# Kernel tuning notes

Hardware: AMD Instinct MI355X
Metric: run time of the kernel (lower is better)

The kernel has to match this reference:

```python
import jax, jax.numpy as jnp
import numpy as np

B, S, D, E, F, TOP_K = 2, 2048, 1024, 8, 4096, 2


def setup_inputs() -> dict:
    key = jax.random.key(0)
    k0, k1, k2, k3 = jax.random.split(key, 4)
    x = jax.random.normal(k0, (B, S, D), dtype=jnp.float32)
    gate_w = jax.random.normal(k1, (D, E), dtype=jnp.float32) * 0.02  # Linear(d_model, num_experts, bias=False)
    w1 = jax.random.normal(k2, (E, D, F), dtype=jnp.float32) * 0.02   # per-expert Linear(d_model, d_ff)
    b1 = jnp.zeros((E, F), dtype=jnp.float32)
    w2 = jax.random.normal(k3, (E, F, D), dtype=jnp.float32) * 0.02   # per-expert Linear(d_ff, d_model)
    b2 = jnp.zeros((E, D), dtype=jnp.float32)
    return {"x": x, "gate_w": gate_w, "w1": w1, "b1": b1, "w2": w2, "b2": b2}


def reference(x, gate_w, w1, b1, w2, b2):
    b, s, d = x.shape
    e = gate_w.shape[1]
    xf = x.reshape(-1, d)                       # [T, D], T = B*S
    t = xf.shape[0]

    # Router: top-k gate scores, softmax over the selected k scores only
    scores = xf @ gate_w                        # [T, E]
    top_v, top_i = jax.lax.top_k(scores, TOP_K)  # [T, K]
    probs = jax.nn.softmax(top_v, axis=-1)       # [T, K]

    # Combine weights per (token, expert); scatter-add of top-k probs.
    combine = jnp.zeros((t, e), dtype=xf.dtype).at[
        jnp.arange(t)[:, None], top_i
    ].add(probs)                                 # [T, E]

    # Dense grouped FFN over all experts (dropout=0 / eval mode -> identity).
    h = jax.nn.gelu(jnp.einsum('td,edf->etf', xf, w1) + b1[:, None, :],
                    approximate=False)           # [E, T, F]
    y = jnp.einsum('etf,efd->etd', h, w2) + b2[:, None, :]  # [E, T, D]

    # Weighted combine: tokens only receive output from their top-k experts.
    out = jnp.einsum('etd,te->td', y, combine)   # [T, D]
    return out.reshape(b, s, d)
```

## Files before the change

### kernel.cpp

```cpp
#include <hip/hip_runtime.h>
#include <math.h>

typedef __bf16 bf16;
typedef __bf16 bf16x8 __attribute__((ext_vector_type(8)));
typedef float f32x4 __attribute__((ext_vector_type(4)));

#define T_TOK 4096
#define D_DIM 1024
#define E_EXP 8
#define F_DIM 4096
#define BM 128
#define BN 128
#define BK 64
#define PAD_SLOTS 9216

__device__ __forceinline__ void gload16(const bf16* g, bf16* l) {
  __builtin_amdgcn_global_load_lds(
      (const __attribute__((address_space(1))) void*)g,
      (__attribute__((address_space(3))) void*)l, 16, 0, 0);
}

__global__ __launch_bounds__(64) void router_kernel(
    const float* __restrict__ x, const float* __restrict__ gw,
    int* __restrict__ eidx, float* __restrict__ pval, int* __restrict__ cnt)
{
  const int t = blockIdx.x;
  const int lane = threadIdx.x;
  const float* xr = x + (size_t)t * D_DIM;
  float s[E_EXP];
#pragma unroll
  for (int e = 0; e < E_EXP; ++e) s[e] = 0.f;
#pragma unroll
  for (int j = 0; j < D_DIM / 64; ++j) {
    const int d = lane * (D_DIM / 64) + j;
    const float xv = xr[d];
    const float* g = gw + (size_t)d * E_EXP;
#pragma unroll
    for (int e = 0; e < E_EXP; ++e) s[e] += xv * g[e];
  }
#pragma unroll
  for (int off = 32; off > 0; off >>= 1) {
#pragma unroll
    for (int e = 0; e < E_EXP; ++e) s[e] += __shfl_xor(s[e], off, 64);
  }
  if (lane == 0) {
    int i0 = 0;
#pragma unroll
    for (int e = 1; e < E_EXP; ++e) if (s[e] > s[i0]) i0 = e;
    int i1 = (i0 == 0) ? 1 : 0;
#pragma unroll
    for (int e = 0; e < E_EXP; ++e) if (e != i0 && s[e] > s[i1]) i1 = e;
    const float p1 = 1.f / (1.f + expf(s[i0] - s[i1]));
    eidx[2 * t] = i0;  eidx[2 * t + 1] = i1;
    pval[2 * t] = 1.f - p1;  pval[2 * t + 1] = p1;
    atomicAdd(&cnt[i0], 1);
    atomicAdd(&cnt[i1], 1);
  }
}

__global__ void prefix_kernel(const int* __restrict__ cnt, int* __restrict__ off,
                              int* __restrict__ cursor)
{
  if (blockIdx.x == 0 && threadIdx.x == 0) {
    int acc = 0;
    for (int e = 0; e < E_EXP; ++e) {
      off[e] = acc;
      cursor[e] = acc;
      acc += ((cnt[e] + BM - 1) / BM) * BM;
    }
    off[E_EXP] = acc;
  }
}

__global__ __launch_bounds__(256) void scatter_kernel(
    const int* __restrict__ eidx, const float* __restrict__ pval,
    int* __restrict__ cursor, int* __restrict__ tok_flat,
    float* __restrict__ prob_flat, int* __restrict__ slot_of)
{
  const int i = blockIdx.x * 256 + threadIdx.x;
  if (i < T_TOK * 2) {
    const int e = eidx[i];
    const int pos = atomicAdd(&cursor[e], 1);
    tok_flat[pos] = i >> 1;
    prob_flat[pos] = pval[i];
    slot_of[i] = pos;
  }
}

__global__ __launch_bounds__(256) void xcast_kernel(const float* __restrict__ x,
                                                    bf16* __restrict__ xb)
{
  const size_t i = (size_t)(blockIdx.x * 256 + threadIdx.x) * 8;
  const float4 a = *(const float4*)(x + i);
  const float4 b = *(const float4*)(x + i + 4);
  union { bf16 v[8]; int4 q; } u;
  u.v[0] = (bf16)a.x; u.v[1] = (bf16)a.y; u.v[2] = (bf16)a.z; u.v[3] = (bf16)a.w;
  u.v[4] = (bf16)b.x; u.v[5] = (bf16)b.y; u.v[6] = (bf16)b.z; u.v[7] = (bf16)b.w;
  *(int4*)(xb + i) = u.q;
}

__global__ __launch_bounds__(256) void wtrans_kernel(const float* __restrict__ src,
                                                     bf16* __restrict__ dst,
                                                     int R, int C)
{
  __shared__ float tile[64][68];
  const int e = blockIdx.z;
  const int r0 = blockIdx.y * 64;
  const int c0 = blockIdx.x * 64;
  const float* sp = src + (size_t)e * R * C;
  const int tr = threadIdx.x >> 4;
  const int tc = (threadIdx.x & 15) * 4;
#pragma unroll
  for (int p = 0; p < 4; ++p) {
    const int r = p * 16 + tr;
    const float4 v = *(const float4*)(sp + (size_t)(r0 + r) * C + c0 + tc);
    *(float4*)&tile[r][tc] = v;
  }
  __syncthreads();
  bf16* dp = dst + (size_t)e * C * R;
  const int oc = threadIdx.x & 31;
  const int orr = (threadIdx.x >> 5) * 8;
#pragma unroll
  for (int p = 0; p < 2; ++p) {
    const int c = p * 32 + oc;
    union { bf16 v[8]; int4 q; } u;
#pragma unroll
    for (int j = 0; j < 8; ++j) u.v[j] = (bf16)tile[orr + j][c];
    *(int4*)(dp + (size_t)(c0 + c) * R + r0 + orr) = u.q;
  }
}

template <int MODE>
__global__ __launch_bounds__(256) void gemm_kernel(
    const bf16* __restrict__ Abase, const bf16* __restrict__ BT,
    const float* __restrict__ bias, const int* __restrict__ cnt,
    const int* __restrict__ off, const int* __restrict__ tok_flat,
    const float* __restrict__ prob_flat, bf16* __restrict__ Hout,
    bf16* __restrict__ Yout)
{
  constexpr int K = (MODE == 0) ? 1024 : 4096;
  constexpr int N = (MODE == 0) ? 4096 : 1024;
  constexpr int NT = N / BN;

  const int b = blockIdx.x;
  const int nt = b % NT;
  const int mt = (b / NT) % 32;
  const int e  = b / (NT * 32);
  if (mt * BM >= cnt[e]) return;
  const int rowBase = off[e] + mt * BM;
  const int nBase = nt * BN;

  __shared__ bf16 sA[BM * BK];
  __shared__ bf16 sB[BN * BK];

  const int tid = threadIdx.x;
  const int lane = tid & 63;
  const int wid = tid >> 6;
  const int mW = (wid >> 1) * 64;
  const int nW = (wid & 1) * 64;

  const bf16* aptr[4];
  const bf16* bptr[4];
#pragma unroll
  for (int j = 0; j < 4; ++j) {
    const int r = wid * 32 + j * 8 + (lane >> 3);
    if (MODE == 0) {
      int tok = tok_flat[rowBase + r];
      if (tok < 0) tok = 0;
      aptr[j] = Abase + (size_t)tok * K + (lane & 7) * 8;
    } else {
      aptr[j] = Abase + (size_t)(rowBase + r) * K + (lane & 7) * 8;
    }
    bptr[j] = BT + ((size_t)e * N + nBase + r) * K + (lane & 7) * 8;
  }

  f32x4 acc[4][4];
#pragma unroll
  for (int m = 0; m < 4; ++m)
#pragma unroll
    for (int n = 0; n < 4; ++n) acc[m][n] = (f32x4){0.f, 0.f, 0.f, 0.f};

  for (int kt = 0; kt < K / BK; ++kt) {
#pragma unroll
    for (int j = 0; j < 4; ++j) {
      gload16(aptr[j] + kt * BK, &sA[(wid * 32 + j * 8) * BK]);
      gload16(bptr[j] + kt * BK, &sB[(wid * 32 + j * 8) * BK]);
    }
    __syncthreads();
#pragma unroll
    for (int ks = 0; ks < 2; ++ks) {
      const int kb = ks * 64 + ((lane >> 4) << 4);
      bf16x8 af[4], bfr[4];
#pragma unroll
      for (int m = 0; m < 4; ++m) {
        const int row = mW + m * 16 + (lane & 15);
        af[m] = *(const bf16x8*)((const char*)sA + row * 128 + kb);
      }
#pragma unroll
      for (int n = 0; n < 4; ++n) {
        const int row = nW + n * 16 + (lane & 15);
        bfr[n] = *(const bf16x8*)((const char*)sB + row * 128 + kb);
      }
#pragma unroll
      for (int m = 0; m < 4; ++m)
#pragma unroll
        for (int n = 0; n < 4; ++n)
          acc[m][n] = __builtin_amdgcn_mfma_f32_16x16x32_bf16(af[m], bfr[n], acc[m][n], 0, 0, 0);
    }
    __syncthreads();
  }

  const int col0 = nW + (lane & 15);
  const int rsub = (lane >> 4) * 4;
  if (MODE == 0) {
#pragma unroll
    for (int m = 0; m < 4; ++m) {
#pragma unroll
      for (int n = 0; n < 4; ++n) {
        const int colg = nBase + col0 + n * 16;
        const float bb = bias[e * N + colg];
#pragma unroll
        for (int r = 0; r < 4; ++r) {
          const int rowl = mW + m * 16 + rsub + r;
          float v = acc[m][n][r] + bb;
          v = 0.5f * v * (1.0f + erff(v * 0.70710678118f));
          Hout[(size_t)(rowBase + rowl) * F_DIM + colg] = (bf16)v;
        }
      }
    }
  } else {
#pragma unroll
    for (int m = 0; m < 4; ++m) {
#pragma unroll
      for (int r = 0; r < 4; ++r) {
        const int slot = rowBase + mW + m * 16 + rsub + r;
        const float p = prob_flat[slot];
#pragma unroll
        for (int n = 0; n < 4; ++n) {
          const int colg = nBase + col0 + n * 16;
          const float v = (acc[m][n][r] + bias[e * N + colg]) * p;
          Yout[(size_t)slot * D_DIM + colg] = (bf16)v;
        }
      }
    }
  }
}

__global__ __launch_bounds__(256) void combine_kernel(
    const bf16* __restrict__ y, const int* __restrict__ slot_of,
    float* __restrict__ out)
{
  const int i = blockIdx.x * 256 + threadIdx.x;
  const int t = i >> 7;
  const int dq = (i & 127) * 8;
  const int s0 = slot_of[2 * t];
  const int s1 = slot_of[2 * t + 1];
  const bf16x8 a = *(const bf16x8*)(y + (size_t)s0 * D_DIM + dq);
  const bf16x8 b = *(const bf16x8*)(y + (size_t)s1 * D_DIM + dq);
  float4 o0, o1;
  o0.x = (float)a[0] + (float)b[0];  o0.y = (float)a[1] + (float)b[1];
  o0.z = (float)a[2] + (float)b[2];  o0.w = (float)a[3] + (float)b[3];
  o1.x = (float)a[4] + (float)b[4];  o1.y = (float)a[5] + (float)b[5];
  o1.z = (float)a[6] + (float)b[6];  o1.w = (float)a[7] + (float)b[7];
  *(float4*)(out + (size_t)t * D_DIM + dq) = o0;
  *(float4*)(out + (size_t)t * D_DIM + dq + 4) = o1;
}

extern "C" void kernel_launch(void* const* d_in, const int* in_sizes, int n_in,
                              void* d_out, int out_size, void* d_ws, size_t ws_size,
                              hipStream_t stream) {
  const float* x      = (const float*)d_in[0];
  const float* gate_w = (const float*)d_in[1];
  const float* w1     = (const float*)d_in[2];
  const float* b1     = (const float*)d_in[3];
  const float* w2     = (const float*)d_in[4];
  const float* b2     = (const float*)d_in[5];
  float* out = (float*)d_out;

  char* ws = (char*)d_ws;
  size_t o = 0;
  bf16* xb  = (bf16*)(ws + o); o += (size_t)T_TOK * D_DIM * 2;
  bf16* h   = (bf16*)(ws + o); o += (size_t)PAD_SLOTS * F_DIM * 2;
  bf16* wT  = (bf16*)(ws + o); o += (size_t)E_EXP * D_DIM * F_DIM * 2;
  bf16* y   = (bf16*)(ws + o); o += (size_t)PAD_SLOTS * D_DIM * 2;
  int*   tok_flat  = (int*)(ws + o);   o += PAD_SLOTS * 4;
  float* prob_flat = (float*)(ws + o); o += PAD_SLOTS * 4;
  int*   slot_of   = (int*)(ws + o);   o += T_TOK * 2 * 4;
  int*   eidx      = (int*)(ws + o);   o += T_TOK * 2 * 4;
  float* pval      = (float*)(ws + o); o += T_TOK * 2 * 4;
  int*   cnt       = (int*)(ws + o);   o += 32;
  int*   cursor    = (int*)(ws + o);   o += 32;
  int*   off       = (int*)(ws + o);   o += 64;

  hipMemsetAsync(cnt, 0, 32, stream);
  hipMemsetAsync(tok_flat, 0xFF, PAD_SLOTS * 4, stream);

  router_kernel<<<T_TOK, 64, 0, stream>>>(x, gate_w, eidx, pval, cnt);
  prefix_kernel<<<1, 64, 0, stream>>>(cnt, off, cursor);
  scatter_kernel<<<(T_TOK * 2) / 256, 256, 0, stream>>>(eidx, pval, cursor,
                                                        tok_flat, prob_flat, slot_of);
  xcast_kernel<<<(T_TOK * D_DIM) / (256 * 8), 256, 0, stream>>>(x, xb);

  wtrans_kernel<<<dim3(F_DIM / 64, D_DIM / 64, E_EXP), 256, 0, stream>>>(w1, wT, D_DIM, F_DIM);
  gemm_kernel<0><<<E_EXP * 32 * (F_DIM / BN), 256, 0, stream>>>(
      xb, wT, b1, cnt, off, tok_flat, prob_flat, h, nullptr);

  wtrans_kernel<<<dim3(D_DIM / 64, F_DIM / 64, E_EXP), 256, 0, stream>>>(w2, wT, F_DIM, D_DIM);
  gemm_kernel<1><<<E_EXP * 32 * (D_DIM / BN), 256, 0, stream>>>(
      h, wT, b2, cnt, off, tok_flat, prob_flat, nullptr, y);

  combine_kernel<<<(T_TOK * D_DIM / 8) / 256, 256, 0, stream>>>(y, slot_of, out);
}
```

Measured before the change: 790.9 us.

## Double-buffer LDS tiles in expert GEMM and remap workgroups per XCD

Splits the GEMM main loop into stage and compute steps with two LDS buffers, so the next K tile is fetched while MFMAs run on the current one, needing one barrier per iteration instead of two. It also remaps block IDs so that consecutive logical tiles land on the same XCD, aiming for better L2 reuse of weight and activation tiles. LDS usage doubles, which can lower occupancy.

```diff
diff --git a/kernel.cpp b/kernel.cpp
--- a/kernel.cpp
+++ b/kernel.cpp
@@ -141,17 +141,23 @@
   constexpr int K = (MODE == 0) ? 1024 : 4096;
   constexpr int N = (MODE == 0) ? 4096 : 1024;
   constexpr int NT = N / BN;
-
-  const int b = blockIdx.x;
-  const int nt = b % NT;
-  const int mt = (b / NT) % 32;
-  const int e  = b / (NT * 32);
+  constexpr int NKT = K / BK;
+
+  const int nwg = E_EXP * 32 * NT;
+  const int orig = blockIdx.x;
+  const int q = nwg >> 3, r = nwg & 7;
+  const int xcd = orig & 7;
+  const int wgid = (xcd < r ? xcd * (q + 1) : r * (q + 1) + (xcd - r) * q) + (orig >> 3);
+
+  const int nt = wgid % NT;
+  const int mt = (wgid / NT) % 32;
+  const int e  = wgid / (NT * 32);
   if (mt * BM >= cnt[e]) return;
   const int rowBase = off[e] + mt * BM;
   const int nBase = nt * BN;
 
-  __shared__ bf16 sA[BM * BK];
-  __shared__ bf16 sB[BN * BK];
+  __shared__ bf16 sA[2][BM * BK];
+  __shared__ bf16 sB[2][BN * BK];
 
   const int tid = threadIdx.x;
   const int lane = tid & 63;
@@ -163,15 +169,15 @@
   const bf16* bptr[4];
 #pragma unroll
   for (int j = 0; j < 4; ++j) {
-    const int r = wid * 32 + j * 8 + (lane >> 3);
+    const int rr = wid * 32 + j * 8 + (lane >> 3);
     if (MODE == 0) {
-      int tok = tok_flat[rowBase + r];
+      int tok = tok_flat[rowBase + rr];
       if (tok < 0) tok = 0;
       aptr[j] = Abase + (size_t)tok * K + (lane & 7) * 8;
     } else {
-      aptr[j] = Abase + (size_t)(rowBase + r) * K + (lane & 7) * 8;
-    }
-    bptr[j] = BT + ((size_t)e * N + nBase + r) * K + (lane & 7) * 8;
+      aptr[j] = Abase + (size_t)(rowBase + rr) * K + (lane & 7) * 8;
+    }
+    bptr[j] = BT + ((size_t)e * N + nBase + rr) * K + (lane & 7) * 8;
   }
 
   f32x4 acc[4][4];
@@ -180,13 +186,16 @@
 #pragma unroll
     for (int n = 0; n < 4; ++n) acc[m][n] = (f32x4){0.f, 0.f, 0.f, 0.f};
 
-  for (int kt = 0; kt < K / BK; ++kt) {
+  auto STAGE = [&](int c, int kt) {
 #pragma unroll
     for (int j = 0; j < 4; ++j) {
-      gload16(aptr[j] + kt * BK, &sA[(wid * 32 + j * 8) * BK]);
-      gload16(bptr[j] + kt * BK, &sB[(wid * 32 + j * 8) * BK]);
-    }
-    __syncthreads();
+      gload16(aptr[j] + kt * BK, &sA[c][(wid * 32 + j * 8) * BK]);
+      gload16(bptr[j] + kt * BK, &sB[c][(wid * 32 + j * 8) * BK]);
+    }
+  };
+  auto COMPUTE = [&](int c) {
+    const char* As = (const char*)sA[c];
+    const char* Bs = (const char*)sB[c];
 #pragma unroll
     for (int ks = 0; ks < 2; ++ks) {
       const int kb = ks * 64 + ((lane >> 4) << 4);
@@ -194,12 +203,12 @@
 #pragma unroll
       for (int m = 0; m < 4; ++m) {
         const int row = mW + m * 16 + (lane & 15);
-        af[m] = *(const bf16x8*)((const char*)sA + row * 128 + kb);
+        af[m] = *(const bf16x8*)(As + row * 128 + kb);
       }
 #pragma unroll
       for (int n = 0; n < 4; ++n) {
         const int row = nW + n * 16 + (lane & 15);
-        bfr[n] = *(const bf16x8*)((const char*)sB + row * 128 + kb);
+        bfr[n] = *(const bf16x8*)(Bs + row * 128 + kb);
       }
 #pragma unroll
       for (int m = 0; m < 4; ++m)
@@ -207,8 +216,18 @@
         for (int n = 0; n < 4; ++n)
           acc[m][n] = __builtin_amdgcn_mfma_f32_16x16x32_bf16(af[m], bfr[n], acc[m][n], 0, 0, 0);
     }
+  };
+
+  STAGE(0, 0);
+  __syncthreads();
+  int cur = 0;
+  for (int kt = 0; kt + 1 < NKT; ++kt) {
+    STAGE(cur ^ 1, kt + 1);
+    COMPUTE(cur);
     __syncthreads();
-  }
+    cur ^= 1;
+  }
+  COMPUTE(cur);
 
   const int col0 = nW + (lane & 15);
   const int rsub = (lane >> 4) * 4;
@@ -220,9 +239,9 @@
         const int colg = nBase + col0 + n * 16;
         const float bb = bias[e * N + colg];
 #pragma unroll
-        for (int r = 0; r < 4; ++r) {
-          const int rowl = mW + m * 16 + rsub + r;
-          float v = acc[m][n][r] + bb;
+        for (int rr = 0; rr < 4; ++rr) {
+          const int rowl = mW + m * 16 + rsub + rr;
+          float v = acc[m][n][rr] + bb;
           v = 0.5f * v * (1.0f + erff(v * 0.70710678118f));
           Hout[(size_t)(rowBase + rowl) * F_DIM + colg] = (bf16)v;
         }
@@ -232,13 +251,13 @@
 #pragma unroll
     for (int m = 0; m < 4; ++m) {
 #pragma unroll
-      for (int r = 0; r < 4; ++r) {
-        const int slot = rowBase + mW + m * 16 + rsub + r;
+      for (int rr = 0; rr < 4; ++rr) {
+        const int slot = rowBase + mW + m * 16 + rsub + rr;
         const float p = prob_flat[slot];
 #pragma unroll
         for (int n = 0; n < 4; ++n) {
           const int colg = nBase + col0 + n * 16;
-          const float v = (acc[m][n][r] + bias[e * N + colg]) * p;
+          const float v = (acc[m][n][rr] + bias[e * N + colg]) * p;
           Yout[(size_t)slot * D_DIM + colg] = (bf16)v;
         }
       }
```

Measured after the change: 874.9 us. 1.11x slower.
